# Optimization experiments

Hardware: AMD Instinct MI355X
Metric: run time of the kernel (lower is better)

Reference implementation:

```python
import jax, jax.numpy as jnp
import numpy as np

PS = 16          # patch_size
E = 256          # embed_dim
NH = 4           # num_heads
THR = 1.5        # entropy_threshold (bits)
LN_EPS = 1e-5


def _ln(x, g, b):
    m = x.mean(-1, keepdims=True)
    v = ((x - m) ** 2).mean(-1, keepdims=True)
    return (x - m) / jnp.sqrt(v + LN_EPS) * g + b


def _forward(video, conv_w, conv_b, wq_w, wq_b, wk_w, wk_b, wv_w, wv_b,
             lnq_g, lnq_b, lnk_g, lnk_b, lnv_g, lnv_b,
             in_proj_w, in_proj_b, out_proj_w, out_proj_b,
             dense_w, dense_b, bproj_w, bproj_b, group_query, ent_table):
    # Conv3d(3->E, k=(3,PS,PS), s=(2,PS,PS), p=(1,0,0)) + ReLU
    x = jax.lax.conv_general_dilated(
        video, conv_w, window_strides=(2, PS, PS),
        padding=((1, 1), (0, 0), (0, 0)),
        dimension_numbers=('NCDHW', 'OIDHW', 'NCDHW'))
    x = jax.nn.relu(x + conv_b[None, :, None, None, None])
    B = x.shape[0]
    tokens = x.reshape(B, E, -1).transpose(0, 2, 1)  # [B, N, E]
    N = tokens.shape[1]

    # per-token byte (no_grad in torch)
    byte = jax.lax.stop_gradient(
        jnp.clip(jnp.round(tokens.mean(-1) * 255.0), 0, 255)).astype(jnp.int32)  # [B, N]
    # entropy predictor: probs = softmax(ent_table[last_byte]) (last byte of running seq)
    logits = ent_table[byte[0]]                      # [N, 256]
    p = jax.nn.softmax(logits, axis=-1)
    ent = -(p * jnp.log2(p + 1e-9)).sum(-1)          # [N]
    boundary = (ent > THR).astype(jnp.int32)
    seg = jnp.cumsum(boundary) - boundary            # exclusive cumsum -> segment id per token

    # DecoderCrossAttention with a single shared group_query per segment
    q0 = jnp.broadcast_to(group_query, (B, 1, E))    # byte_representations
    query = _ln(q0 @ wq_w.T + wq_b, lnq_g, lnq_b)    # [B,1,E]
    k = _ln(tokens @ wk_w.T + wk_b, lnk_g, lnk_b)    # [B,N,E]
    v = _ln(tokens @ wv_w.T + wv_b, lnv_g, lnv_b)

    Wqi, Wki, Wvi = in_proj_w[:E], in_proj_w[E:2 * E], in_proj_w[2 * E:]
    bqi, bki, bvi = in_proj_b[:E], in_proj_b[E:2 * E], in_proj_b[2 * E:]
    dh = E // NH
    qp = ((query @ Wqi.T + bqi) * (dh ** -0.5)).reshape(B, NH, dh)  # [B,H,dh]
    kp = (k @ Wki.T + bki).reshape(B, N, NH, dh)
    vp = (v @ Wvi.T + bvi).reshape(B, N, NH, dh)

    scores = jnp.einsum('bhd,bnhd->nbh', qp, kp)     # [N,B,H]
    smax = jax.ops.segment_max(scores, seg, num_segments=N)   # [N,B,H]
    w = jnp.exp(scores - smax[seg])
    denom = jax.ops.segment_sum(w, seg, num_segments=N)       # [N,B,H]
    num = jax.ops.segment_sum(w[..., None] * vp.transpose(1, 0, 2, 3),
                              seg, num_segments=N)            # [N,B,H,dh]
    count = jax.ops.segment_sum(jnp.ones((N,), scores.dtype), seg, num_segments=N)
    valid = count > 0
    safe = jnp.where(valid[:, None, None], denom, 1.0)
    attn = (num / safe[..., None]).transpose(1, 0, 2, 3).reshape(B, N, E)
    out = attn @ out_proj_w.T + out_proj_b
    out = out @ dense_w.T + dense_b
    out = out + q0                                   # residual with byte_representations
    patches = out @ bproj_w.T + bproj_b              # binary_proj
    return jnp.where(valid[None, :, None], patches, 0.0)  # [B, N, E] padded


def setup_inputs() -> dict:
    key = jax.random.key(0)
    ks = jax.random.split(key, 16)
    rn = lambda k, s, sc=0.02: jax.random.normal(k, s, jnp.float32) * sc
    z = lambda *s: jnp.zeros(s, jnp.float32)
    o = lambda *s: jnp.ones(s, jnp.float32)
    return {
        'video': jax.random.normal(ks[0], (4, 3, 32, 224, 224), jnp.float32),
        'conv_w': rn(ks[1], (E, 3, 3, PS, PS)), 'conv_b': z(E),
        'wq_w': rn(ks[2], (E, E)), 'wq_b': z(E),
        'wk_w': rn(ks[3], (E, E)), 'wk_b': z(E),
        'wv_w': rn(ks[4], (E, E)), 'wv_b': z(E),
        'lnq_g': o(E), 'lnq_b': z(E),
        'lnk_g': o(E), 'lnk_b': z(E),
        'lnv_g': o(E), 'lnv_b': z(E),
        'in_proj_w': rn(ks[5], (3 * E, E)), 'in_proj_b': z(3 * E),
        'out_proj_w': rn(ks[6], (E, E)), 'out_proj_b': z(E),
        'dense_w': rn(ks[7], (E, E)), 'dense_b': z(E),
        'bproj_w': rn(ks[8], (E, E)), 'bproj_b': z(E),
        'group_query': jax.random.normal(ks[9], (1, 1, E), jnp.float32),
        'ent_table': jax.random.normal(ks[10], (256, 256), jnp.float32) * 6.0,
    }


def reference(video, conv_w, conv_b, wq_w, wq_b, wk_w, wk_b, wv_w, wv_b,
              lnq_g, lnq_b, lnk_g, lnk_b, lnv_g, lnv_b,
              in_proj_w, in_proj_b, out_proj_w, out_proj_b,
              dense_w, dense_b, bproj_w, bproj_b, group_query, ent_table):
    return _forward(video, conv_w, conv_b, wq_w, wq_b, wk_w, wk_b, wv_w, wv_b,
                    lnq_g, lnq_b, lnk_g, lnk_b, lnv_g, lnv_b,
                    in_proj_w, in_proj_b, out_proj_w, out_proj_b,
                    dense_w, dense_b, bproj_w, bproj_b, group_query, ent_table)
```

## Files before the change

kernel.cpp:

```cpp
#include <hip/hip_runtime.h>
#include <hip/hip_bf16.h>
#include <math.h>

#define NTOK 3136
#define MT 12544
#define KCV 2304
#define THRESH 1.5f
#define LN_EPS 1e-5f

typedef short short8 __attribute__((ext_vector_type(8)));
typedef float f32x4 __attribute__((ext_vector_type(4)));

__device__ __forceinline__ unsigned short f2bf(float f) {
    unsigned int u = __float_as_uint(f);
    u += 0x7fffu + ((u >> 16) & 1u);
    return (unsigned short)(u >> 16);
}
__device__ __forceinline__ float bf2f(unsigned short h) {
    return __uint_as_float(((unsigned int)h) << 16);
}
__device__ __forceinline__ unsigned int cvt_pk_bf16(float x0, float x1) {
    union { __hip_bfloat162 h; unsigned int u; } cv;
    cv.h = __float22bfloat162_rn(make_float2(x0, x1));
    return cv.u;
}
__device__ __forceinline__ void async16(const void* g, void* l) {
    __builtin_amdgcn_global_load_lds((const __attribute__((address_space(1))) void*)g,
                                     (__attribute__((address_space(3))) void*)l, 16, 0, 0);
}

__device__ __forceinline__ float wsum(float v) {
#pragma unroll
    for (int o = 32; o > 0; o >>= 1) v += __shfl_xor(v, o);
    return v;
}
__device__ __forceinline__ float wmax(float v) {
#pragma unroll
    for (int o = 32; o > 0; o >>= 1) v = fmaxf(v, __shfl_xor(v, o));
    return v;
}

__global__ __launch_bounds__(256) void prep_k(
    const float* __restrict__ cw, unsigned short* __restrict__ cwh,
    unsigned short* __restrict__ cwl,
    const float* __restrict__ s0, const float* __restrict__ s1, const float* __restrict__ s2,
    const float* __restrict__ s3, const float* __restrict__ s4, const float* __restrict__ s5,
    unsigned short* __restrict__ dst,
    const float* __restrict__ gq, const float* __restrict__ wq_w,
    const float* __restrict__ wq_b, const float* __restrict__ lnq_g,
    const float* __restrict__ lnq_b, const float* __restrict__ inW,
    const float* __restrict__ inB, float* __restrict__ qp)
{
    const int blk = blockIdx.x;
    if (blk < 288) {
        int i = blk * 256 + threadIdx.x;
        int e = i & 255, kg = i >> 8;
        const float4* sp = (const float4*)(cw + (size_t)e * KCV + kg * 8);
        float4 x0 = sp[0], x1 = sp[1];
        float av[8] = {x0.x, x0.y, x0.z, x0.w, x1.x, x1.y, x1.z, x1.w};
        short8 hh, ll;
#pragma unroll
        for (int j = 0; j < 8; ++j) {
            unsigned short h = f2bf(av[j]);
            hh[j] = (short)h;
            ll[j] = (short)f2bf(av[j] - bf2f(h));
        }
        size_t off = (size_t)kg * 2048 + e * 8;
        *(short8*)&cwh[off] = hh;
        *(short8*)&cwl[off] = ll;
    } else if (blk < 2336) {
        int i = (blk - 288) * 256 + threadIdx.x;
        if (i >= 524288) return;
        float v;
        if      (i <  65536) v = s0[i];
        else if (i < 131072) v = s1[i - 65536];
        else if (i < 327680) v = s2[i - 131072];
        else if (i < 393216) v = s3[i - 327680];
        else if (i < 458752) v = s4[i - 393216];
        else                 v = s5[i - 458752];
        dst[i] = f2bf(v);
    } else {
        __shared__ float sh[256];
        __shared__ float red[256];
        const int t = threadIdx.x;
        float acc = wq_b[t];
        for (int j = 0; j < 256; j++) acc += gq[j] * wq_w[t * 256 + j];
        red[t] = acc; __syncthreads();
        for (int o = 128; o > 0; o >>= 1) { if (t < o) red[t] += red[t + o]; __syncthreads(); }
        float m = red[0] * (1.f / 256.f);
        __syncthreads();
        float d = acc - m;
        red[t] = d * d; __syncthreads();
        for (int o = 128; o > 0; o >>= 1) { if (t < o) red[t] += red[t + o]; __syncthreads(); }
        float inv = 1.f / sqrtf(red[0] * (1.f / 256.f) + LN_EPS);
        sh[t] = d * inv * lnq_g[t] + lnq_b[t];
        __syncthreads();
        float a2 = inB[t];
        for (int j = 0; j < 256; j++) a2 += sh[j] * inW[t * 256 + j];
        qp[t] = a2 * 0.125f;
    }
}

__global__ __launch_bounds__(256) void conv_mfma_k(
    const float* __restrict__ video, const unsigned short* __restrict__ cwh,
    const unsigned short* __restrict__ cwl, const float* __restrict__ cbias,
    float* __restrict__ tokmean4, unsigned short* __restrict__ outB)
{
    __shared__ __align__(16) unsigned short Bh[8192], Bl[8192];
    const int t    = threadIdx.x;
    const int lane = t & 63;
    const int w    = t >> 6;
    const int l15  = lane & 15, lq = lane >> 4;
    const int v_  = blockIdx.x;
    const int s_  = (v_ & 7) * 98 + (v_ >> 3);
    const int mb  = s_ >> 2, eb = s_ & 3;
    const int m0  = mb * 64, e0 = eb * 64;

    const int m = m0 + w * 16 + l15;
    const int b = m / NTOK, n = m % NTOK;
    const int d = n / 196, hw = n % 196;
    const int h = hw / 14, ww = hw % 14;
    const float* vb = video + (size_t)(b * 3) * (32 * 50176) + (h * 16) * 224 + ww * 16;
    const int dbase = 2 * d - 1;

    f32x4 acc[4] = {};
    float4 a0, a1, a2, a3, b0, b1, b2, b3;
    short8 rh0, rh1, rl0, rl1;

#define BLOAD(s)                                                                     \
    {                                                                                \
        const size_t g0 = (size_t)((s) * 8 + w) * 2048 + (e0 + lane) * 8;            \
        const size_t g1 = g0 + 4 * 2048;                                             \
        rh0 = *(const short8*)(cwh + g0);                                            \
        rh1 = *(const short8*)(cwh + g1);                                            \
        rl0 = *(const short8*)(cwl + g0);                                            \
        rl1 = *(const short8*)(cwl + g1);                                            \
    }
#define BSTORE(buf)                                                                  \
    {                                                                                \
        const int o = (buf) * 4096 + w * 512 + lane * 8;                             \
        *(short8*)&Bh[o]        = rh0;                                               \
        *(short8*)&Bh[o + 2048] = rh1;                                               \
        *(short8*)&Bl[o]        = rl0;                                               \
        *(short8*)&Bl[o + 2048] = rl1;                                               \
    }
#define LOAD_A32(k0v, x0, x1)                                                        \
    {                                                                                \
        const int k0  = (k0v) + lq * 8;                                              \
        const int c   = k0 / 768;                                                    \
        const int rem = k0 - c * 768;                                                \
        const int kd  = rem >> 8;                                                    \
        const int r2  = rem & 255;                                                   \
        const int id  = dbase + kd;                                                  \
        x0 = make_float4(0.f, 0.f, 0.f, 0.f); x1 = x0;                               \
        if (id >= 0) {                                                               \
            const float* p = vb + (size_t)c * (32 * 50176) + id * 50176 +            \
                             (r2 >> 4) * 224 + (r2 & 15);                            \
            x0 = *(const float4*)p;                                                  \
            x1 = *(const float4*)(p + 4);                                            \
        }                                                                            \
    }
#define CVT_AB(y0, y1, fah, fal)                                                     \
    short8 fah, fal;                                                                 \
    {                                                                                \
        float av[8] = {y0.x, y0.y, y0.z, y0.w, y1.x, y1.y, y1.z, y1.w};              \
        unsigned int ph[4], pl[4];                                                   \
        _Pragma("unroll")                                                            \
        for (int j = 0; j < 4; ++j) {                                                \
            float u0 = av[2 * j], u1 = av[2 * j + 1];                                \
            unsigned int hu = cvt_pk_bf16(u0, u1);                                   \
            float r0 = u0 - __uint_as_float(hu << 16);                               \
            float r1 = u1 - __uint_as_float(hu & 0xffff0000u);                       \
            ph[j] = hu;                                                              \
            pl[j] = cvt_pk_bf16(r0, r1);                                             \
        }                                                                            \
        int4 phv = make_int4(ph[0], ph[1], ph[2], ph[3]);                            \
        int4 plv = make_int4(pl[0], pl[1], pl[2], pl[3]);                            \
        fah = *(short8*)&phv;                                                        \
        fal = *(short8*)&plv;                                                        \
    }

    BLOAD(0);
    LOAD_A32(0, a0, a1);
    LOAD_A32(32, a2, a3);
    BSTORE(0);
    __syncthreads();

    for (int s = 0; s < 36; ++s) {
        const int cbuf = s & 1;
        if (s + 1 < 36) {
            BLOAD(s + 1);
            LOAD_A32((s + 1) * 64,      b0, b1);
            LOAD_A32((s + 1) * 64 + 32, b2, b3);
        }
        {
            CVT_AB(a0, a1, fah, fal);
            const int rb = cbuf * 4096 + lq * 512 + l15 * 8;
#pragma unroll
            for (int ct = 0; ct < 4; ++ct) {
                short8 fbh = *(const short8*)&Bh[rb + ct * 128];
                short8 fbl = *(const short8*)&Bl[rb + ct * 128];
                acc[ct] = __builtin_amdgcn_mfma_f32_16x16x32_bf16(fah, fbh, acc[ct], 0, 0, 0);
                acc[ct] = __builtin_amdgcn_mfma_f32_16x16x32_bf16(fah, fbl, acc[ct], 0, 0, 0);
                acc[ct] = __builtin_amdgcn_mfma_f32_16x16x32_bf16(fal, fbh, acc[ct], 0, 0, 0);
            }
        }
        {
            CVT_AB(a2, a3, fah, fal);
            const int rb = cbuf * 4096 + (4 + lq) * 512 + l15 * 8;
#pragma unroll
            for (int ct = 0; ct < 4; ++ct) {
                short8 fbh = *(const short8*)&Bh[rb + ct * 128];
                short8 fbl = *(const short8*)&Bl[rb + ct * 128];
                acc[ct] = __builtin_amdgcn_mfma_f32_16x16x32_bf16(fah, fbh, acc[ct], 0, 0, 0);
                acc[ct] = __builtin_amdgcn_mfma_f32_16x16x32_bf16(fah, fbl, acc[ct], 0, 0, 0);
                acc[ct] = __builtin_amdgcn_mfma_f32_16x16x32_bf16(fal, fbh, acc[ct], 0, 0, 0);
            }
        }
        if (s + 1 < 36) BSTORE(cbuf ^ 1);
        __syncthreads();
        a0 = b0; a1 = b1; a2 = b2; a3 = b3;
    }
#undef BLOAD
#undef BSTORE
#undef LOAD_A32
#undef CVT_AB

    const int rbase = m0 + w * 16 + lq * 4;
    float rsum[4] = {0.f, 0.f, 0.f, 0.f};
#pragma unroll
    for (int ct = 0; ct < 4; ++ct) {
        int e = e0 + ct * 16 + l15;
        float bias = cbias[e];
#pragma unroll
        for (int r = 0; r < 4; ++r) {
            float vv = fmaxf(acc[ct][r] + bias, 0.f);
            outB[(size_t)(rbase + r) * 256 + e] = f2bf(vv);
            rsum[r] += vv;
        }
    }
    if (m0 < NTOK) {
#pragma unroll
        for (int r = 0; r < 4; ++r) {
            float sv = rsum[r];
            sv += __shfl_xor(sv, 1); sv += __shfl_xor(sv, 2);
            sv += __shfl_xor(sv, 4); sv += __shfl_xor(sv, 8);
            if (l15 == 0) tokmean4[(size_t)eb * NTOK + rbase + r] = sv;
        }
    }
}

__global__ __launch_bounds__(256) void gemm_single_k(
    const unsigned short* __restrict__ A, const unsigned short* __restrict__ W,
    const float* __restrict__ bias, const float* __restrict__ addvec,
    const int* __restrict__ Sptr, float* __restrict__ outF, unsigned short* __restrict__ outB)
{
    __shared__ __align__(16) unsigned short As[8192], Bs[8192];
    const int t = threadIdx.x, lane = t & 63, w = t >> 6;
    const int v_ = blockIdx.x;
    const int s_ = (v_ & 7) * 98 + (v_ >> 3);
    const int m0 = (s_ >> 2) * 64, e0 = (s_ & 3) * 64;
    const int l15 = lane & 15, lq = lane >> 4;
    const unsigned short* ga = A + (size_t)(m0 + lane) * 256;
    const unsigned short* gb = W + (size_t)(e0 + lane) * 256;
#pragma unroll
    for (int kg = w; kg < 16; kg += 4) {
        async16(ga + kg * 8, &As[kg * 512]);
        async16(gb + kg * 8, &Bs[kg * 512]);
    }
    f32x4 acc[4] = {};
    __syncthreads();
#pragma unroll
    for (int s = 0; s < 4; ++s) {
        int kg = s * 4 + lq;
        short8 a = *(const short8*)&As[kg * 512 + (w * 16 + l15) * 8];
#pragma unroll
        for (int ct = 0; ct < 4; ++ct) {
            short8 bb = *(const short8*)&Bs[kg * 512 + (ct * 16 + l15) * 8];
            acc[ct] = __builtin_amdgcn_mfma_f32_16x16x32_bf16(a, bb, acc[ct], 0, 0, 0);
        }
    }
    __syncthreads();
#pragma unroll
    for (int kg = w; kg < 16; kg += 4) {
        async16(ga + (16 + kg) * 8, &As[kg * 512]);
        async16(gb + (16 + kg) * 8, &Bs[kg * 512]);
    }
    __syncthreads();
#pragma unroll
    for (int s = 0; s < 4; ++s) {
        int kg = s * 4 + lq;
        short8 a = *(const short8*)&As[kg * 512 + (w * 16 + l15) * 8];
#pragma unroll
        for (int ct = 0; ct < 4; ++ct) {
            short8 bb = *(const short8*)&Bs[kg * 512 + (ct * 16 + l15) * 8];
            acc[ct] = __builtin_amdgcn_mfma_f32_16x16x32_bf16(a, bb, acc[ct], 0, 0, 0);
        }
    }
    int S = Sptr ? *Sptr : 0x7fffffff;
    int rbase = m0 + w * 16 + lq * 4;
#pragma unroll
    for (int ct = 0; ct < 4; ++ct) {
        int e = e0 + ct * 16 + l15;
        float bv = bias[e] + (addvec ? addvec[e] : 0.f);
#pragma unroll
        for (int r = 0; r < 4; ++r) {
            int mm = rbase + r;
            float vv = acc[ct][r] + bv;
            if ((mm % NTOK) >= S) vv = 0.f;
            size_t off = (size_t)mm * 256 + e;
            if (outF) outF[off] = vv;
            if (outB) outB[off] = f2bf(vv);
        }
    }
}

__global__ __launch_bounds__(256) void gemm_dual_k(
    const unsigned short* __restrict__ A0, const unsigned short* __restrict__ A1,
    const unsigned short* __restrict__ W,
    const float* __restrict__ bias0, const float* __restrict__ bias1,
    unsigned short* __restrict__ outB0, unsigned short* __restrict__ outB1,
    const float* __restrict__ qp, float* __restrict__ sc)
{
    __shared__ __align__(16) unsigned short As[8192], Bs[8192];
    const int t = threadIdx.x, lane = t & 63, w = t >> 6;
    const int v_ = blockIdx.x;
    const int s_ = (v_ & 7) * 196 + (v_ >> 3);
    const int mb = s_ >> 3, ebg = s_ & 7;
    const int half = ebg >> 2;
    const unsigned short* A = half ? A1 : A0;
    const float* bias = half ? bias1 : bias0;
    unsigned short* outB = half ? outB1 : outB0;
    const int m0 = mb * 64, eg0 = ebg * 64, el0 = (ebg & 3) * 64;
    const int l15 = lane & 15, lq = lane >> 4;
    const unsigned short* ga = A + (size_t)(m0 + lane) * 256;
    const unsigned short* gb = W + (size_t)(eg0 + lane) * 256;
#pragma unroll
    for (int kg = w; kg < 16; kg += 4) {
        async16(ga + kg * 8, &As[kg * 512]);
        async16(gb + kg * 8, &Bs[kg * 512]);
    }
    f32x4 acc[4] = {};
    __syncthreads();
#pragma unroll
    for (int s = 0; s < 4; ++s) {
        int kg = s * 4 + lq;
        short8 a = *(const short8*)&As[kg * 512 + (w * 16 + l15) * 8];
#pragma unroll
        for (int ct = 0; ct < 4; ++ct) {
            short8 bb = *(const short8*)&Bs[kg * 512 + (ct * 16 + l15) * 8];
            acc[ct] = __builtin_amdgcn_mfma_f32_16x16x32_bf16(a, bb, acc[ct], 0, 0, 0);
        }
    }
    __syncthreads();
#pragma unroll
    for (int kg = w; kg < 16; kg += 4) {
        async16(ga + (16 + kg) * 8, &As[kg * 512]);
        async16(gb + (16 + kg) * 8, &Bs[kg * 512]);
    }
    __syncthreads();
#pragma unroll
    for (int s = 0; s < 4; ++s) {
        int kg = s * 4 + lq;
        short8 a = *(const short8*)&As[kg * 512 + (w * 16 + l15) * 8];
#pragma unroll
        for (int ct = 0; ct < 4; ++ct) {
            short8 bb = *(const short8*)&Bs[kg * 512 + (ct * 16 + l15) * 8];
            acc[ct] = __builtin_amdgcn_mfma_f32_16x16x32_bf16(a, bb, acc[ct], 0, 0, 0);
        }
    }
    int rbase = m0 + w * 16 + lq * 4;
    if (qp && half == 0) {
        float sp[4] = {0.f, 0.f, 0.f, 0.f};
#pragma unroll
        for (int ct = 0; ct < 4; ++ct) {
            int e = el0 + ct * 16 + l15;
            float bv = bias[e];
            float qv = qp[e];
#pragma unroll
            for (int r = 0; r < 4; ++r) sp[r] += (acc[ct][r] + bv) * qv;
        }
#pragma unroll
        for (int r = 0; r < 4; ++r) {
            sp[r] += __shfl_xor(sp[r], 1); sp[r] += __shfl_xor(sp[r], 2);
            sp[r] += __shfl_xor(sp[r], 4); sp[r] += __shfl_xor(sp[r], 8);
        }
        if (l15 == 0) {
#pragma unroll
            for (int r = 0; r < 4; ++r) {
                int mm = rbase + r;
                int bb = mm / NTOK, nn = mm % NTOK;
                sc[(bb * 4 + ebg) * NTOK + nn] = sp[r];
            }
        }
    } else {
#pragma unroll
        for (int ct = 0; ct < 4; ++ct) {
            int e = el0 + ct * 16 + l15;
            float bv = bias[e];
#pragma unroll
            for (int r = 0; r < 4; ++r) {
                float vv = acc[ct][r] + bv;
                outB[(size_t)(rbase + r) * 256 + e] = f2bf(vv);
            }
        }
    }
}

__global__ __launch_bounds__(256) void boundary_k(
    const float* __restrict__ tokmean4, const float* __restrict__ ent_table,
    int* __restrict__ boundary)
{
    int n    = blockIdx.x * 4 + (threadIdx.x >> 6);
    int lane = threadIdx.x & 63;
    float s0 = tokmean4[n];
    float s1 = tokmean4[NTOK + n];
    float s2 = tokmean4[2 * NTOK + n];
    float s3 = tokmean4[3 * NTOK + n];
    float mean = ((s0 + s1) + (s2 + s3)) * (1.f / 256.f);
    float bf = rintf(mean * 255.f);
    bf = fminf(fmaxf(bf, 0.f), 255.f);
    int byte = (int)bf;
    const float4 lg = reinterpret_cast<const float4*>(ent_table + byte * 256)[lane];
    float mx = wmax(fmaxf(fmaxf(lg.x, lg.y), fmaxf(lg.z, lg.w)));
    float e0 = expf(lg.x - mx), e1 = expf(lg.y - mx), e2 = expf(lg.z - mx), e3 = expf(lg.w - mx);
    float z = wsum(e0 + e1 + e2 + e3);
    float iz = 1.f / z;
    float p0 = e0 * iz, p1 = e1 * iz, p2 = e2 * iz, p3 = e3 * iz;
    float ep = -(p0 * log2f(p0 + 1e-9f) + p1 * log2f(p1 + 1e-9f) +
                 p2 * log2f(p2 + 1e-9f) + p3 * log2f(p3 + 1e-9f));
    ep = wsum(ep);
    if (lane == 0) boundary[n] = (ep > THRESH) ? 1 : 0;
}

__global__ __launch_bounds__(256) void scan_k(const int* __restrict__ boundary,
    int* __restrict__ seg_start, int* __restrict__ Sptr)
{
    __shared__ int sums[256];
    const int t = threadIdx.x;
    const int CH = 13;
    int base = t * CH;
    int s = 0;
    for (int i = 0; i < CH; i++) { int n = base + i; if (n < NTOK) s += boundary[n]; }
    sums[t] = s; __syncthreads();
    for (int o = 1; o < 256; o <<= 1) {
        int v = sums[t];
        int u = (t >= o) ? sums[t - o] : 0;
        __syncthreads();
        sums[t] = v + u;
        __syncthreads();
    }
    int run = (t == 0) ? 0 : sums[t - 1];
    if (t == 0) seg_start[0] = 0;
    for (int i = 0; i < CH; i++) {
        int n = base + i;
        if (n >= NTOK) break;
        int v = boundary[n];
        if (n == NTOK - 1) { Sptr[0] = run + 1; seg_start[run + 1] = NTOK; }
        if (v && (n + 1 < NTOK)) seg_start[run + 1] = n + 1;
        run += v;
    }
}

__global__ __launch_bounds__(256) void lnKV_k(
    const unsigned short* __restrict__ Pk, const unsigned short* __restrict__ Pv,
    const float* __restrict__ gk, const float* __restrict__ bk,
    const float* __restrict__ gv, const float* __restrict__ bv,
    unsigned short* __restrict__ Yk, unsigned short* __restrict__ Yv)
{
    int row  = blockIdx.x * 4 + (threadIdx.x >> 6);
    int lane = threadIdx.x & 63;
    int half = row >= MT;
    int r    = half ? row - MT : row;
    const unsigned short* X = half ? Pv : Pk;
    const float* g = half ? gv : gk;
    const float* b = half ? bv : bk;
    unsigned short* Y = half ? Yv : Yk;
    ushort4 xr = reinterpret_cast<const ushort4*>(X + (size_t)r * 256)[lane];
    float x0 = bf2f(xr.x), x1 = bf2f(xr.y), x2 = bf2f(xr.z), x3 = bf2f(xr.w);
    float m = wsum(x0 + x1 + x2 + x3) * (1.f / 256.f);
    float d0 = x0 - m, d1 = x1 - m, d2 = x2 - m, d3 = x3 - m;
    float var = wsum(d0 * d0 + d1 * d1 + d2 * d2 + d3 * d3) * (1.f / 256.f);
    float inv = 1.f / sqrtf(var + LN_EPS);
    float4 g4 = reinterpret_cast<const float4*>(g)[lane];
    float4 b4 = reinterpret_cast<const float4*>(b)[lane];
    ushort4 y;
    y.x = f2bf(d0 * inv * g4.x + b4.x);
    y.y = f2bf(d1 * inv * g4.y + b4.y);
    y.z = f2bf(d2 * inv * g4.z + b4.z);
    y.w = f2bf(d3 * inv * g4.w + b4.w);
    reinterpret_cast<ushort4*>(Y + (size_t)r * 256)[lane] = y;
}

__global__ __launch_bounds__(256) void attn_bf_k(const float* __restrict__ sc,
    const unsigned short* __restrict__ vp, const int* __restrict__ seg_start,
    const int* __restrict__ Sptr, unsigned short* __restrict__ attn)
{
    int s    = blockIdx.x;
    int b    = blockIdx.y;
    int h    = threadIdx.x >> 6;
    int lane = threadIdx.x & 63;
    unsigned short* orow = attn + ((size_t)b * NTOK + s) * 256;
    int S = *Sptr;
    if (s >= S) { orow[h * 64 + lane] = 0; return; }
    int st = seg_start[s], en = seg_start[s + 1];
    const float* scr = sc + (b * 4 + h) * NTOK;
    float m = -1e30f;
    for (int n = st; n < en; n++) m = fmaxf(m, scr[n]);
    float den = 0.f, acc = 0.f;
    const unsigned short* vpb = vp + (size_t)b * NTOK * 256 + h * 64 + lane;
    for (int n = st; n < en; n++) {
        float wgt = expf(scr[n] - m);
        den += wgt;
        acc += wgt * bf2f(vpb[(size_t)n * 256]);
    }
    orow[h * 64 + lane] = f2bf(acc / den);
}

extern "C" void kernel_launch(void* const* d_in, const int* in_sizes, int n_in,
                              void* d_out, int out_size, void* d_ws, size_t ws_size,
                              hipStream_t stream)
{
    const float* video      = (const float*)d_in[0];
    const float* conv_w     = (const float*)d_in[1];
    const float* conv_b     = (const float*)d_in[2];
    const float* wq_w       = (const float*)d_in[3];
    const float* wq_b       = (const float*)d_in[4];
    const float* wk_w       = (const float*)d_in[5];
    const float* wk_b       = (const float*)d_in[6];
    const float* wv_w       = (const float*)d_in[7];
    const float* wv_b       = (const float*)d_in[8];
    const float* lnq_g      = (const float*)d_in[9];
    const float* lnq_b      = (const float*)d_in[10];
    const float* lnk_g      = (const float*)d_in[11];
    const float* lnk_b      = (const float*)d_in[12];
    const float* lnv_g      = (const float*)d_in[13];
    const float* lnv_b      = (const float*)d_in[14];
    const float* in_proj_w  = (const float*)d_in[15];
    const float* in_proj_b  = (const float*)d_in[16];
    const float* out_proj_w = (const float*)d_in[17];
    const float* out_proj_b = (const float*)d_in[18];
    const float* dense_w    = (const float*)d_in[19];
    const float* dense_b    = (const float*)d_in[20];
    const float* bproj_w    = (const float*)d_in[21];
    const float* bproj_b    = (const float*)d_in[22];
    const float* group_q    = (const float*)d_in[23];
    const float* ent_table  = (const float*)d_in[24];
    float* out = (float*)d_out;

    float* tokmean4 = (float*)d_ws;
    unsigned short* Pk  = (unsigned short*)(tokmean4 + 16384);
    unsigned short* Pv  = Pk  + (size_t)MT * 256;
    unsigned short* B1  = Pv  + (size_t)MT * 256;
    unsigned short* B2k = B1  + (size_t)MT * 256;
    unsigned short* B2v = B2k + (size_t)MT * 256;
    unsigned short* B3v = B2v + (size_t)MT * 256;
    unsigned short* cwh = B3v + (size_t)MT * 256;
    unsigned short* cwl = cwh + 256 * KCV;
    unsigned short* wpool = cwl + 256 * KCV;
    float* sc = (float*)(wpool + 524288);
    float* qp = sc + 16 * NTOK;
    int* boundary  = (int*)(qp + 256);
    int* seg_start = boundary + NTOK;
    int* Sp        = seg_start + (NTOK + 1);

    const unsigned short* inpb   = wpool + 131072;
    const unsigned short* outpb  = wpool + 327680;
    const unsigned short* denseb = wpool + 393216;
    const unsigned short* bprojb = wpool + 458752;

    dim3 blk(256);
    prep_k<<<dim3(2337), blk, 0, stream>>>(conv_w, cwh, cwl,
                                           wk_w, wv_w, in_proj_w, out_proj_w,
                                           dense_w, bproj_w, wpool,
                                           group_q, wq_w, wq_b, lnq_g, lnq_b,
                                           in_proj_w, in_proj_b, qp);
    conv_mfma_k<<<dim3(784), blk, 0, stream>>>(video, cwh, cwl, conv_b, tokmean4, B1);
    boundary_k<<<dim3(NTOK / 4), blk, 0, stream>>>(tokmean4, ent_table, boundary);
    scan_k<<<dim3(1), blk, 0, stream>>>(boundary, seg_start, Sp);
    gemm_dual_k<<<dim3(1568), blk, 0, stream>>>(B1, B1, wpool, wk_b, wv_b, Pk, Pv,
                                                nullptr, nullptr);
    lnKV_k<<<dim3(2 * MT / 4), blk, 0, stream>>>(Pk, Pv, lnk_g, lnk_b, lnv_g, lnv_b,
                                                 B2k, B2v);
    gemm_dual_k<<<dim3(1568), blk, 0, stream>>>(B2k, B2v, inpb + 65536,
                                                in_proj_b + 256, in_proj_b + 512,
                                                nullptr, B3v, qp, sc);
    attn_bf_k<<<dim3(NTOK, 4), blk, 0, stream>>>(sc, B3v, seg_start, Sp, B1);
    gemm_single_k<<<dim3(784), blk, 0, stream>>>(B1, outpb, out_proj_b,
                                                 nullptr, nullptr, nullptr, B2k);
    gemm_single_k<<<dim3(784), blk, 0, stream>>>(B2k, denseb, dense_b,
                                                 group_q, nullptr, nullptr, B2v);
    gemm_single_k<<<dim3(784), blk, 0, stream>>>(B2v, bprojb, bproj_b,
                                                 nullptr, Sp, out, nullptr);
}
```

Baseline: 329.3 us.

## Switch conv kernel to 32x32x16 MFMA with 2x2 wave tiling

Rewrites the conv implicit-GEMM kernel so each wave computes a 32x32 output tile with 32x32x16 bf16 MFMA, instead of a 16x64 strip built from 16x16x32 MFMAs. The B tile layout in LDS and the A loads are reorganised to match, and per-token partial sums are now written in eight column slices, so the boundary kernel reads eight partials. Launch bounds request 3 blocks per CU. The goal is fewer LDS fragment reads per MFMA and better MFMA throughput, at the cost of more registers per thread for the prefetched A data and a changed epilogue store pattern.

```diff
diff --git a/kernel.cpp b/kernel.cpp
--- a/kernel.cpp
+++ b/kernel.cpp
@@ -10,6 +10,7 @@
 
 typedef short short8 __attribute__((ext_vector_type(8)));
 typedef float f32x4 __attribute__((ext_vector_type(4)));
+typedef float f32x16 __attribute__((ext_vector_type(16)));
 
 __device__ __forceinline__ unsigned short f2bf(float f) {
     unsigned int u = __float_as_uint(f);
@@ -101,52 +102,53 @@
     }
 }
 
-__global__ __launch_bounds__(256) void conv_mfma_k(
+__global__ __launch_bounds__(256, 3) void conv_mfma_k(
     const float* __restrict__ video, const unsigned short* __restrict__ cwh,
     const unsigned short* __restrict__ cwl, const float* __restrict__ cbias,
-    float* __restrict__ tokmean4, unsigned short* __restrict__ outB)
+    float* __restrict__ tokmean8, unsigned short* __restrict__ outB)
 {
     __shared__ __align__(16) unsigned short Bh[8192], Bl[8192];
     const int t    = threadIdx.x;
     const int lane = t & 63;
     const int w    = t >> 6;
-    const int l15  = lane & 15, lq = lane >> 4;
+    const int l31  = lane & 31, lh = lane >> 5;
+    const int wr   = w >> 1,    wc = w & 1;
     const int v_  = blockIdx.x;
     const int s_  = (v_ & 7) * 98 + (v_ >> 3);
     const int mb  = s_ >> 2, eb = s_ & 3;
     const int m0  = mb * 64, e0 = eb * 64;
 
-    const int m = m0 + w * 16 + l15;
+    const int m = m0 + wr * 32 + l31;
     const int b = m / NTOK, n = m % NTOK;
     const int d = n / 196, hw = n % 196;
     const int h = hw / 14, ww = hw % 14;
     const float* vb = video + (size_t)(b * 3) * (32 * 50176) + (h * 16) * 224 + ww * 16;
     const int dbase = 2 * d - 1;
 
-    f32x4 acc[4] = {};
-    float4 a0, a1, a2, a3, b0, b1, b2, b3;
+    f32x16 acc = {};
+    float4 a0, a1, a2, a3, a4, a5, a6, a7;
+    float4 n0, n1, n2, n3, n4, n5, n6, n7;
     short8 rh0, rh1, rl0, rl1;
 
 #define BLOAD(s)                                                                     \
     {                                                                                \
-        const size_t g0 = (size_t)((s) * 8 + w) * 2048 + (e0 + lane) * 8;            \
-        const size_t g1 = g0 + 4 * 2048;                                             \
+        const size_t g0 = (size_t)((s) * 8 + (t >> 5)) * 2048 + (e0 + (t & 31) * 2) * 8; \
         rh0 = *(const short8*)(cwh + g0);                                            \
-        rh1 = *(const short8*)(cwh + g1);                                            \
+        rh1 = *(const short8*)(cwh + g0 + 8);                                        \
         rl0 = *(const short8*)(cwl + g0);                                            \
-        rl1 = *(const short8*)(cwl + g1);                                            \
+        rl1 = *(const short8*)(cwl + g0 + 8);                                        \
     }
 #define BSTORE(buf)                                                                  \
     {                                                                                \
-        const int o = (buf) * 4096 + w * 512 + lane * 8;                             \
-        *(short8*)&Bh[o]        = rh0;                                               \
-        *(short8*)&Bh[o + 2048] = rh1;                                               \
-        *(short8*)&Bl[o]        = rl0;                                               \
-        *(short8*)&Bl[o + 2048] = rl1;                                               \
-    }
-#define LOAD_A32(k0v, x0, x1)                                                        \
+        const int o = (buf) * 4096 + (t >> 5) * 512 + (t & 31) * 16;                 \
+        *(short8*)&Bh[o]     = rh0;                                                  \
+        *(short8*)&Bh[o + 8] = rh1;                                                  \
+        *(short8*)&Bl[o]     = rl0;                                                  \
+        *(short8*)&Bl[o + 8] = rl1;                                                  \
+    }
+#define LOAD_OCT(kv, x0, x1)                                                         \
     {                                                                                \
-        const int k0  = (k0v) + lq * 8;                                              \
+        const int k0  = (kv) + lh * 8;                                               \
         const int c   = k0 / 768;                                                    \
         const int rem = k0 - c * 768;                                                \
         const int kd  = rem >> 8;                                                    \
@@ -179,10 +181,22 @@
         fah = *(short8*)&phv;                                                        \
         fal = *(short8*)&plv;                                                        \
     }
+#define KCHUNK(i, ya, yb, cbuf)                                                      \
+    {                                                                                \
+        CVT_AB(ya, yb, fah, fal);                                                    \
+        const int rb = (cbuf) * 4096 + ((2 * (i) + lh) * 64 + wc * 32 + l31) * 8;    \
+        short8 fbh = *(const short8*)&Bh[rb];                                        \
+        short8 fbl = *(const short8*)&Bl[rb];                                        \
+        acc = __builtin_amdgcn_mfma_f32_32x32x16_bf16(fah, fbh, acc, 0, 0, 0);       \
+        acc = __builtin_amdgcn_mfma_f32_32x32x16_bf16(fah, fbl, acc, 0, 0, 0);       \
+        acc = __builtin_amdgcn_mfma_f32_32x32x16_bf16(fal, fbh, acc, 0, 0, 0);       \
+    }
 
     BLOAD(0);
-    LOAD_A32(0, a0, a1);
-    LOAD_A32(32, a2, a3);
+    LOAD_OCT(0,  a0, a1);
+    LOAD_OCT(16, a2, a3);
+    LOAD_OCT(32, a4, a5);
+    LOAD_OCT(48, a6, a7);
     BSTORE(0);
     __syncthreads();
 
@@ -190,63 +204,42 @@
         const int cbuf = s & 1;
         if (s + 1 < 36) {
             BLOAD(s + 1);
-            LOAD_A32((s + 1) * 64,      b0, b1);
-            LOAD_A32((s + 1) * 64 + 32, b2, b3);
-        }
-        {
-            CVT_AB(a0, a1, fah, fal);
-            const int rb = cbuf * 4096 + lq * 512 + l15 * 8;
-#pragma unroll
-            for (int ct = 0; ct < 4; ++ct) {
-                short8 fbh = *(const short8*)&Bh[rb + ct * 128];
-                short8 fbl = *(const short8*)&Bl[rb + ct * 128];
-                acc[ct] = __builtin_amdgcn_mfma_f32_16x16x32_bf16(fah, fbh, acc[ct], 0, 0, 0);
-                acc[ct] = __builtin_amdgcn_mfma_f32_16x16x32_bf16(fah, fbl, acc[ct], 0, 0, 0);
-                acc[ct] = __builtin_amdgcn_mfma_f32_16x16x32_bf16(fal, fbh, acc[ct], 0, 0, 0);
-            }
-        }
-        {
-            CVT_AB(a2, a3, fah, fal);
-            const int rb = cbuf * 4096 + (4 + lq) * 512 + l15 * 8;
-#pragma unroll
-            for (int ct = 0; ct < 4; ++ct) {
-                short8 fbh = *(const short8*)&Bh[rb + ct * 128];
-                short8 fbl = *(const short8*)&Bl[rb + ct * 128];
-                acc[ct] = __builtin_amdgcn_mfma_f32_16x16x32_bf16(fah, fbh, acc[ct], 0, 0, 0);
-                acc[ct] = __builtin_amdgcn_mfma_f32_16x16x32_bf16(fah, fbl, acc[ct], 0, 0, 0);
-                acc[ct] = __builtin_amdgcn_mfma_f32_16x16x32_bf16(fal, fbh, acc[ct], 0, 0, 0);
-            }
-        }
+            const int kb = (s + 1) * 64;
+            LOAD_OCT(kb,      n0, n1);
+            LOAD_OCT(kb + 16, n2, n3);
+            LOAD_OCT(kb + 32, n4, n5);
+            LOAD_OCT(kb + 48, n6, n7);
+        }
+        KCHUNK(0, a0, a1, cbuf);
+        KCHUNK(1, a2, a3, cbuf);
+        KCHUNK(2, a4, a5, cbuf);
+        KCHUNK(3, a6, a7, cbuf);
         if (s + 1 < 36) BSTORE(cbuf ^ 1);
         __syncthreads();
-        a0 = b0; a1 = b1; a2 = b2; a3 = b3;
+        a0 = n0; a1 = n1; a2 = n2; a3 = n3;
+        a4 = n4; a5 = n5; a6 = n6; a7 = n7;
     }
 #undef BLOAD
 #undef BSTORE
-#undef LOAD_A32
+#undef LOAD_OCT
 #undef CVT_AB
-
-    const int rbase = m0 + w * 16 + lq * 4;
-    float rsum[4] = {0.f, 0.f, 0.f, 0.f};
-#pragma unroll
-    for (int ct = 0; ct < 4; ++ct) {
-        int e = e0 + ct * 16 + l15;
-        float bias = cbias[e];
-#pragma unroll
-        for (int r = 0; r < 4; ++r) {
-            float vv = fmaxf(acc[ct][r] + bias, 0.f);
-            outB[(size_t)(rbase + r) * 256 + e] = f2bf(vv);
-            rsum[r] += vv;
-        }
-    }
-    if (m0 < NTOK) {
-#pragma unroll
-        for (int r = 0; r < 4; ++r) {
-            float sv = rsum[r];
-            sv += __shfl_xor(sv, 1); sv += __shfl_xor(sv, 2);
-            sv += __shfl_xor(sv, 4); sv += __shfl_xor(sv, 8);
-            if (l15 == 0) tokmean4[(size_t)eb * NTOK + rbase + r] = sv;
-        }
+#undef KCHUNK
+
+    const int e = e0 + wc * 32 + l31;
+    const float bias = cbias[e];
+    const bool emit_tm = (m0 < NTOK);
+#pragma unroll
+    for (int r = 0; r < 16; ++r) {
+        int row = (r & 3) + 8 * (r >> 2) + 4 * lh;
+        int mm  = m0 + wr * 32 + row;
+        float vv = fmaxf(acc[r] + bias, 0.f);
+        outB[(size_t)mm * 256 + e] = f2bf(vv);
+        float sv = vv;
+        sv += __shfl_xor(sv, 1); sv += __shfl_xor(sv, 2);
+        sv += __shfl_xor(sv, 4); sv += __shfl_xor(sv, 8);
+        sv += __shfl_xor(sv, 16);
+        if (emit_tm && l31 == 0)
+            tokmean8[(size_t)(eb * 2 + wc) * NTOK + mm] = sv;
     }
 }
 
@@ -408,16 +401,20 @@
 }
 
 __global__ __launch_bounds__(256) void boundary_k(
-    const float* __restrict__ tokmean4, const float* __restrict__ ent_table,
+    const float* __restrict__ tokmean8, const float* __restrict__ ent_table,
     int* __restrict__ boundary)
 {
     int n    = blockIdx.x * 4 + (threadIdx.x >> 6);
     int lane = threadIdx.x & 63;
-    float s0 = tokmean4[n];
-    float s1 = tokmean4[NTOK + n];
-    float s2 = tokmean4[2 * NTOK + n];
-    float s3 = tokmean4[3 * NTOK + n];
-    float mean = ((s0 + s1) + (s2 + s3)) * (1.f / 256.f);
+    float s0 = tokmean8[n];
+    float s1 = tokmean8[NTOK + n];
+    float s2 = tokmean8[2 * NTOK + n];
+    float s3 = tokmean8[3 * NTOK + n];
+    float s4 = tokmean8[4 * NTOK + n];
+    float s5 = tokmean8[5 * NTOK + n];
+    float s6 = tokmean8[6 * NTOK + n];
+    float s7 = tokmean8[7 * NTOK + n];
+    float mean = (((s0 + s1) + (s2 + s3)) + ((s4 + s5) + (s6 + s7))) * (1.f / 256.f);
     float bf = rintf(mean * 255.f);
     bf = fminf(fmaxf(bf, 0.f), 255.f);
     int byte = (int)bf;
@@ -548,8 +545,8 @@
     const float* ent_table  = (const float*)d_in[24];
     float* out = (float*)d_out;
 
-    float* tokmean4 = (float*)d_ws;
-    unsigned short* Pk  = (unsigned short*)(tokmean4 + 16384);
+    float* tokmean8 = (float*)d_ws;
+    unsigned short* Pk  = (unsigned short*)(tokmean8 + 32768);
     unsigned short* Pv  = Pk  + (size_t)MT * 256;
     unsigned short* B1  = Pv  + (size_t)MT * 256;
     unsigned short* B2k = B1  + (size_t)MT * 256;
@@ -575,8 +572,8 @@
                                            dense_w, bproj_w, wpool,
                                            group_q, wq_w, wq_b, lnq_g, lnq_b,
                                            in_proj_w, in_proj_b, qp);
-    conv_mfma_k<<<dim3(784), blk, 0, stream>>>(video, cwh, cwl, conv_b, tokmean4, B1);
-    boundary_k<<<dim3(NTOK / 4), blk, 0, stream>>>(tokmean4, ent_table, boundary);
+    conv_mfma_k<<<dim3(784), blk, 0, stream>>>(video, cwh, cwl, conv_b, tokmean8, B1);
+    boundary_k<<<dim3(NTOK / 4), blk, 0, stream>>>(tokmean8, ent_table, boundary);
     scan_k<<<dim3(1), blk, 0, stream>>>(boundary, seg_start, Sp);
     gemm_dual_k<<<dim3(1568), blk, 0, stream>>>(B1, B1, wpool, wk_b, wv_b, Pk, Pv,
                                                 nullptr, nullptr);
```

New measurement: 361.9 us. +9.9%, slower.

## Fold out/dense/bproj linears into one weight and fuse LayerNorm into in-proj GEMM

Applied to the files above, without the earlier changes.

Precomputes a combined weight Wb·Wd·Wo and matching bias on device, so the chain of three linear GEMMs after attention becomes one GEMM. It also removes the separate LayerNorm pass over K/V by computing row statistics inside the in-projection GEMM and normalizing the A tile before the MFMA. This cuts two large GEMM launches, one elementwise kernel, and their intermediate traffic. In exchange it adds small fp32 weight-product prep kernels each call and a different rounding order (bf16 composite weights, single-pass variance).

```diff
diff --git a/kernel.cpp b/kernel.cpp
--- a/kernel.cpp
+++ b/kernel.cpp
@@ -44,16 +44,19 @@
     const float* __restrict__ cw, unsigned short* __restrict__ cwh,
     unsigned short* __restrict__ cwl,
     const float* __restrict__ s0, const float* __restrict__ s1, const float* __restrict__ s2,
-    const float* __restrict__ s3, const float* __restrict__ s4, const float* __restrict__ s5,
     unsigned short* __restrict__ dst,
     const float* __restrict__ gq, const float* __restrict__ wq_w,
     const float* __restrict__ wq_b, const float* __restrict__ lnq_g,
     const float* __restrict__ lnq_b, const float* __restrict__ inW,
-    const float* __restrict__ inB, float* __restrict__ qp)
+    const float* __restrict__ inB, float* __restrict__ qp,
+    const float* __restrict__ Wd, const float* __restrict__ Wo,
+    const float* __restrict__ bo, const float* __restrict__ bd,
+    float* __restrict__ D1, float* __restrict__ tvec)
 {
     const int blk = blockIdx.x;
+    const int t = threadIdx.x;
     if (blk < 288) {
-        int i = blk * 256 + threadIdx.x;
+        int i = blk * 256 + t;
         int e = i & 255, kg = i >> 8;
         const float4* sp = (const float4*)(cw + (size_t)e * KCV + kg * 8);
         float4 x0 = sp[0], x1 = sp[1];
@@ -68,21 +71,17 @@
         size_t off = (size_t)kg * 2048 + e * 8;
         *(short8*)&cwh[off] = hh;
         *(short8*)&cwl[off] = ll;
-    } else if (blk < 2336) {
-        int i = (blk - 288) * 256 + threadIdx.x;
-        if (i >= 524288) return;
+    } else if (blk < 1568) {
+        int i = (blk - 288) * 256 + t;
+        if (i >= 327680) return;
         float v;
         if      (i <  65536) v = s0[i];
         else if (i < 131072) v = s1[i - 65536];
-        else if (i < 327680) v = s2[i - 131072];
-        else if (i < 393216) v = s3[i - 327680];
-        else if (i < 458752) v = s4[i - 393216];
-        else                 v = s5[i - 458752];
+        else                 v = s2[i - 131072];
         dst[i] = f2bf(v);
-    } else {
+    } else if (blk == 1568) {
         __shared__ float sh[256];
         __shared__ float red[256];
-        const int t = threadIdx.x;
         float acc = wq_b[t];
         for (int j = 0; j < 256; j++) acc += gq[j] * wq_w[t * 256 + j];
         red[t] = acc; __syncthreads();
@@ -98,6 +97,34 @@
         float a2 = inB[t];
         for (int j = 0; j < 256; j++) a2 += sh[j] * inW[t * 256 + j];
         qp[t] = a2 * 0.125f;
+    } else if (blk < 1825) {
+        int i = blk - 1569;
+        float acc = 0.f;
+        for (int k = 0; k < 256; k++) acc += Wd[i * 256 + k] * Wo[k * 256 + t];
+        D1[i * 256 + t] = acc;
+    } else {
+        float acc = bd[t] + gq[t];
+        for (int k = 0; k < 256; k++) acc += Wd[t * 256 + k] * bo[k];
+        tvec[t] = acc;
+    }
+}
+
+__global__ __launch_bounds__(256) void prep2_k(
+    const float* __restrict__ Wb, const float* __restrict__ D1,
+    const float* __restrict__ tvec, const float* __restrict__ bb,
+    unsigned short* __restrict__ WcB, float* __restrict__ bc)
+{
+    const int blk = blockIdx.x;
+    const int t = threadIdx.x;
+    if (blk < 256) {
+        int i = blk;
+        float acc = 0.f;
+        for (int k = 0; k < 256; k++) acc += Wb[i * 256 + k] * D1[k * 256 + t];
+        WcB[i * 256 + t] = f2bf(acc);
+    } else {
+        float acc = bb[t];
+        for (int k = 0; k < 256; k++) acc += Wb[t * 256 + k] * tvec[k];
+        bc[t] = acc;
     }
 }
 
@@ -319,8 +346,7 @@
     const unsigned short* __restrict__ A0, const unsigned short* __restrict__ A1,
     const unsigned short* __restrict__ W,
     const float* __restrict__ bias0, const float* __restrict__ bias1,
-    unsigned short* __restrict__ outB0, unsigned short* __restrict__ outB1,
-    const float* __restrict__ qp, float* __restrict__ sc)
+    unsigned short* __restrict__ outB0, unsigned short* __restrict__ outB1)
 {
     __shared__ __align__(16) unsigned short As[8192], Bs[8192];
     const int t = threadIdx.x, lane = t & 63, w = t >> 6;
@@ -370,7 +396,104 @@
         }
     }
     int rbase = m0 + w * 16 + lq * 4;
-    if (qp && half == 0) {
+#pragma unroll
+    for (int ct = 0; ct < 4; ++ct) {
+        int e = el0 + ct * 16 + l15;
+        float bv = bias[e];
+#pragma unroll
+        for (int r = 0; r < 4; ++r) {
+            float vv = acc[ct][r] + bv;
+            outB[(size_t)(rbase + r) * 256 + e] = f2bf(vv);
+        }
+    }
+}
+
+__global__ __launch_bounds__(256, 2) void gemm_ln_k(
+    const unsigned short* __restrict__ A0, const unsigned short* __restrict__ A1,
+    const unsigned short* __restrict__ W,
+    const float* __restrict__ bias0, const float* __restrict__ bias1,
+    const float* __restrict__ g0, const float* __restrict__ b0,
+    const float* __restrict__ g1, const float* __restrict__ b1,
+    unsigned short* __restrict__ outVp, const float* __restrict__ qp,
+    float* __restrict__ sc)
+{
+    __shared__ __align__(16) unsigned short As[16384], Bs[16384];
+    __shared__ float pst[2][4][64];
+    __shared__ float rmean[64], rinv[64];
+    const int t = threadIdx.x, lane = t & 63, w = t >> 6;
+    const int v_ = blockIdx.x;
+    const int s_ = (v_ & 7) * 196 + (v_ >> 3);
+    const int mb = s_ >> 3, ebg = s_ & 7;
+    const int half = ebg >> 2;
+    const unsigned short* A = half ? A1 : A0;
+    const float* bias = half ? bias1 : bias0;
+    const float* lng  = half ? g1 : g0;
+    const float* lnb  = half ? b1 : b0;
+    const int m0 = mb * 64, eg0 = ebg * 64, el0 = (ebg & 3) * 64;
+    const int l15 = lane & 15, lq = lane >> 4;
+    const unsigned short* ga = A + (size_t)(m0 + lane) * 256;
+    const unsigned short* gb = W + (size_t)(eg0 + lane) * 256;
+#pragma unroll
+    for (int kg = w; kg < 32; kg += 4) {
+        async16(ga + kg * 8, &As[kg * 512]);
+        async16(gb + kg * 8, &Bs[kg * 512]);
+    }
+    __syncthreads();
+    {
+        float sum = 0.f, sq = 0.f;
+#pragma unroll
+        for (int k8 = 0; k8 < 8; ++k8) {
+            short8 x = *(const short8*)&As[(w * 8 + k8) * 512 + lane * 8];
+#pragma unroll
+            for (int j = 0; j < 8; ++j) {
+                float xv = bf2f((unsigned short)x[j]);
+                sum += xv; sq += xv * xv;
+            }
+        }
+        pst[0][w][lane] = sum; pst[1][w][lane] = sq;
+    }
+    __syncthreads();
+    if (w == 0) {
+        float s4 = (pst[0][0][lane] + pst[0][1][lane]) + (pst[0][2][lane] + pst[0][3][lane]);
+        float q4 = (pst[1][0][lane] + pst[1][1][lane]) + (pst[1][2][lane] + pst[1][3][lane]);
+        float mean = s4 * (1.f / 256.f);
+        float var  = q4 * (1.f / 256.f) - mean * mean;
+        rmean[lane] = mean;
+        rinv[lane]  = 1.f / sqrtf(var + LN_EPS);
+    }
+    __syncthreads();
+    const float myMean = rmean[w * 16 + l15];
+    const float myInv  = rinv [w * 16 + l15];
+
+    f32x4 acc[4] = {};
+#pragma unroll
+    for (int s = 0; s < 8; ++s) {
+        int kg = s * 4 + lq;
+        short8 araw = *(const short8*)&As[kg * 512 + (w * 16 + l15) * 8];
+        float4 gA = *(const float4*)&lng[kg * 8];
+        float4 gB = *(const float4*)&lng[kg * 8 + 4];
+        float4 bA = *(const float4*)&lnb[kg * 8];
+        float4 bB = *(const float4*)&lnb[kg * 8 + 4];
+        float y[8];
+        y[0] = (bf2f((unsigned short)araw[0]) - myMean) * myInv * gA.x + bA.x;
+        y[1] = (bf2f((unsigned short)araw[1]) - myMean) * myInv * gA.y + bA.y;
+        y[2] = (bf2f((unsigned short)araw[2]) - myMean) * myInv * gA.z + bA.z;
+        y[3] = (bf2f((unsigned short)araw[3]) - myMean) * myInv * gA.w + bA.w;
+        y[4] = (bf2f((unsigned short)araw[4]) - myMean) * myInv * gB.x + bB.x;
+        y[5] = (bf2f((unsigned short)araw[5]) - myMean) * myInv * gB.y + bB.y;
+        y[6] = (bf2f((unsigned short)araw[6]) - myMean) * myInv * gB.z + bB.z;
+        y[7] = (bf2f((unsigned short)araw[7]) - myMean) * myInv * gB.w + bB.w;
+        int4 pk = make_int4(cvt_pk_bf16(y[0], y[1]), cvt_pk_bf16(y[2], y[3]),
+                            cvt_pk_bf16(y[4], y[5]), cvt_pk_bf16(y[6], y[7]));
+        short8 a = *(short8*)&pk;
+#pragma unroll
+        for (int ct = 0; ct < 4; ++ct) {
+            short8 bb = *(const short8*)&Bs[kg * 512 + (ct * 16 + l15) * 8];
+            acc[ct] = __builtin_amdgcn_mfma_f32_16x16x32_bf16(a, bb, acc[ct], 0, 0, 0);
+        }
+    }
+    int rbase = m0 + w * 16 + lq * 4;
+    if (half == 0) {
         float sp[4] = {0.f, 0.f, 0.f, 0.f};
 #pragma unroll
         for (int ct = 0; ct < 4; ++ct) {
@@ -401,7 +524,7 @@
 #pragma unroll
             for (int r = 0; r < 4; ++r) {
                 float vv = acc[ct][r] + bv;
-                outB[(size_t)(rbase + r) * 256 + e] = f2bf(vv);
+                outVp[(size_t)(rbase + r) * 256 + e] = f2bf(vv);
             }
         }
     }
@@ -460,36 +583,6 @@
         if (v && (n + 1 < NTOK)) seg_start[run + 1] = n + 1;
         run += v;
     }
-}
-
-__global__ __launch_bounds__(256) void lnKV_k(
-    const unsigned short* __restrict__ Pk, const unsigned short* __restrict__ Pv,
-    const float* __restrict__ gk, const float* __restrict__ bk,
-    const float* __restrict__ gv, const float* __restrict__ bv,
-    unsigned short* __restrict__ Yk, unsigned short* __restrict__ Yv)
-{
-    int row  = blockIdx.x * 4 + (threadIdx.x >> 6);
-    int lane = threadIdx.x & 63;
-    int half = row >= MT;
-    int r    = half ? row - MT : row;
-    const unsigned short* X = half ? Pv : Pk;
-    const float* g = half ? gv : gk;
-    const float* b = half ? bv : bk;
-    unsigned short* Y = half ? Yv : Yk;
-    ushort4 xr = reinterpret_cast<const ushort4*>(X + (size_t)r * 256)[lane];
-    float x0 = bf2f(xr.x), x1 = bf2f(xr.y), x2 = bf2f(xr.z), x3 = bf2f(xr.w);
-    float m = wsum(x0 + x1 + x2 + x3) * (1.f / 256.f);
-    float d0 = x0 - m, d1 = x1 - m, d2 = x2 - m, d3 = x3 - m;
-    float var = wsum(d0 * d0 + d1 * d1 + d2 * d2 + d3 * d3) * (1.f / 256.f);
-    float inv = 1.f / sqrtf(var + LN_EPS);
-    float4 g4 = reinterpret_cast<const float4*>(g)[lane];
-    float4 b4 = reinterpret_cast<const float4*>(b)[lane];
-    ushort4 y;
-    y.x = f2bf(d0 * inv * g4.x + b4.x);
-    y.y = f2bf(d1 * inv * g4.y + b4.y);
-    y.z = f2bf(d2 * inv * g4.z + b4.z);
-    y.w = f2bf(d3 * inv * g4.w + b4.w);
-    reinterpret_cast<ushort4*>(Y + (size_t)r * 256)[lane] = y;
 }
 
 __global__ __launch_bounds__(256) void attn_bf_k(const float* __restrict__ sc,
@@ -552,9 +645,7 @@
     unsigned short* Pk  = (unsigned short*)(tokmean4 + 16384);
     unsigned short* Pv  = Pk  + (size_t)MT * 256;
     unsigned short* B1  = Pv  + (size_t)MT * 256;
-    unsigned short* B2k = B1  + (size_t)MT * 256;
-    unsigned short* B2v = B2k + (size_t)MT * 256;
-    unsigned short* B3v = B2v + (size_t)MT * 256;
+    unsigned short* B3v = B1  + (size_t)MT * 256;
     unsigned short* cwh = B3v + (size_t)MT * 256;
     unsigned short* cwl = cwh + 256 * KCV;
     unsigned short* wpool = cwl + 256 * KCV;
@@ -563,33 +654,30 @@
     int* boundary  = (int*)(qp + 256);
     int* seg_start = boundary + NTOK;
     int* Sp        = seg_start + (NTOK + 1);
-
-    const unsigned short* inpb   = wpool + 131072;
-    const unsigned short* outpb  = wpool + 327680;
-    const unsigned short* denseb = wpool + 393216;
-    const unsigned short* bprojb = wpool + 458752;
+    float* D1   = (float*)(Sp + 64);
+    float* tvec = D1 + 65536;
+    float* bc   = tvec + 256;
+
+    const unsigned short* inpb = wpool + 131072;
+    unsigned short* WcB        = wpool + 327680;
 
     dim3 blk(256);
-    prep_k<<<dim3(2337), blk, 0, stream>>>(conv_w, cwh, cwl,
-                                           wk_w, wv_w, in_proj_w, out_proj_w,
-                                           dense_w, bproj_w, wpool,
+    prep_k<<<dim3(1826), blk, 0, stream>>>(conv_w, cwh, cwl,
+                                           wk_w, wv_w, in_proj_w, wpool,
                                            group_q, wq_w, wq_b, lnq_g, lnq_b,
-                                           in_proj_w, in_proj_b, qp);
+                                           in_proj_w, in_proj_b, qp,
+                                           dense_w, out_proj_w, out_proj_b, dense_b,
+                                           D1, tvec);
+    prep2_k<<<dim3(257), blk, 0, stream>>>(bproj_w, D1, tvec, bproj_b, WcB, bc);
     conv_mfma_k<<<dim3(784), blk, 0, stream>>>(video, cwh, cwl, conv_b, tokmean4, B1);
     boundary_k<<<dim3(NTOK / 4), blk, 0, stream>>>(tokmean4, ent_table, boundary);
     scan_k<<<dim3(1), blk, 0, stream>>>(boundary, seg_start, Sp);
-    gemm_dual_k<<<dim3(1568), blk, 0, stream>>>(B1, B1, wpool, wk_b, wv_b, Pk, Pv,
-                                                nullptr, nullptr);
-    lnKV_k<<<dim3(2 * MT / 4), blk, 0, stream>>>(Pk, Pv, lnk_g, lnk_b, lnv_g, lnv_b,
-                                                 B2k, B2v);
-    gemm_dual_k<<<dim3(1568), blk, 0, stream>>>(B2k, B2v, inpb + 65536,
-                                                in_proj_b + 256, in_proj_b + 512,
-                                                nullptr, B3v, qp, sc);
+    gemm_dual_k<<<dim3(1568), blk, 0, stream>>>(B1, B1, wpool, wk_b, wv_b, Pk, Pv);
+    gemm_ln_k<<<dim3(1568), blk, 0, stream>>>(Pk, Pv, inpb + 65536,
+                                              in_proj_b + 256, in_proj_b + 512,
+                                              lnk_g, lnk_b, lnv_g, lnv_b,
+                                              B3v, qp, sc);
     attn_bf_k<<<dim3(NTOK, 4), blk, 0, stream>>>(sc, B3v, seg_start, Sp, B1);
-    gemm_single_k<<<dim3(784), blk, 0, stream>>>(B1, outpb, out_proj_b,
-                                                 nullptr, nullptr, nullptr, B2k);
-    gemm_single_k<<<dim3(784), blk, 0, stream>>>(B2k, denseb, dense_b,
-                                                 group_q, nullptr, nullptr, B2v);
-    gemm_single_k<<<dim3(784), blk, 0, stream>>>(B2v, bprojb, bproj_b,
+    gemm_single_k<<<dim3(784), blk, 0, stream>>>(B1, WcB, bc,
                                                  nullptr, Sp, out, nullptr);
 }
```

Result: no change. 323.0 us (-1.9%).
